# Performance work log

Measured on AMD Instinct MI355X. Metric: run time of the kernel, lower is better.

Reference implementation:

```python
import jax, jax.numpy as jnp
import numpy as np

EPS = 1e-12  # torch F.normalize eps


def setup_inputs() -> dict:
    key = jax.random.key(0)
    ks = jax.random.split(key, 6)
    B, D, F, N, C, L = 4096, 1024, 1024, 8192, 64, 28
    features = jax.random.normal(ks[0], (B, D), dtype=jnp.float32)
    labels = (jax.random.uniform(ks[1], (B, L)) < 0.2).astype(jnp.float32)  # multi-label targets
    g_weight = jax.random.normal(ks[2], (F, D), dtype=jnp.float32) * 0.02  # nn.Linear weight [out,in]
    ex_features = jax.random.normal(ks[3], (N, D), dtype=jnp.float32)
    ex_class_reps = jax.random.uniform(ks[4], (N, C), dtype=jnp.float32) * 2.0 - 1.0
    class_reps = jax.random.uniform(ks[5], (L, C), dtype=jnp.float32) * 2.0 - 1.0
    return {"features": features, "labels": labels, "g_weight": g_weight,
            "ex_features": ex_features, "ex_class_reps": ex_class_reps,
            "class_reps": class_reps, "p_factor": 3}


def _l2norm(x):
    # torch F.normalize(dim=1): x / max(||x||_2, eps)
    n = jnp.sqrt(jnp.sum(x * x, axis=1, keepdims=True))
    return x / jnp.maximum(n, EPS)


def reference(features, labels, g_weight, ex_features, ex_class_reps, class_reps, p_factor):
    # g projection (bias=False)
    f = features @ g_weight.T            # [B, F]
    exf = ex_features @ g_weight.T       # [N, F]
    # cosine similarity: normalized matmul
    s = _l2norm(f) @ _l2norm(exf).T      # [B, N]
    # power-sign activation
    a = jnp.sign(s) * jnp.abs(s) ** p_factor
    # L1 normalize along exemplar axis
    a = a / jnp.maximum(jnp.sum(jnp.abs(a), axis=1, keepdims=True), EPS)
    # exemplar readout
    echo = a @ ex_class_reps             # [B, C]
    # cdist (euclidean) to class representatives -> negative distances as logits
    diff = echo[:, None, :] - class_reps[None, :, :]   # [B, L, C]
    neg_dists = -jnp.sqrt(jnp.sum(diff * diff, axis=-1))  # [B, L]
    # BCEWithLogitsLoss (mean reduction)
    x, y = neg_dists, labels
    loss = jnp.mean(jnp.maximum(x, 0.0) - x * y + jnp.log1p(jnp.exp(-jnp.abs(x))))
    return (loss, neg_dists)
```

## Files before the change

### kernel.cpp

```cpp
#include <hip/hip_runtime.h>
#include <math.h>

#define EPSN 1e-12f

typedef __attribute__((ext_vector_type(8))) short short8;
typedef __attribute__((ext_vector_type(4))) float f32x4;

__device__ __forceinline__ void split_hi_lo(float x, unsigned short& h, unsigned short& l)
{
    unsigned int xb = __float_as_uint(x);
    h = (unsigned short)(xb >> 16);
    float r = x - __uint_as_float(xb & 0xffff0000u);
    l = (unsigned short)(__float_as_uint(r) >> 16);
}

__device__ __forceinline__ unsigned short f2bf_rne(float x)
{
    unsigned int u = __float_as_uint(x);
    unsigned int r = u + 0x7fffu + ((u >> 16) & 1u);
    return (unsigned short)(r >> 16);
}

__device__ __forceinline__ void gload16(const void* g, void* l)
{
    __builtin_amdgcn_global_load_lds(
        (const __attribute__((address_space(1))) void*)g,
        (__attribute__((address_space(3))) void*)l, 16, 0, 0);
}

__device__ __forceinline__ short8 read_frag(const unsigned char* plane, int row, int chunk)
{
    int byte = row * 128 + ((chunk ^ (row & 7)) << 4);
    return *reinterpret_cast<const short8*>(plane + byte);
}

__device__ __forceinline__ void stage_split(const float* __restrict__ src, int K, int k0,
                                            unsigned char* hi_plane, unsigned char* lo_plane,
                                            int tid)
{
#pragma unroll
    for (int q = 0; q < 8; ++q) {
        int idx = tid + q * 256;
        int row = idx >> 4;
        int f4  = idx & 15;
        float4 v = *reinterpret_cast<const float4*>(&src[(size_t)row * K + k0 + f4 * 4]);
        unsigned short h[4], l[4];
        split_hi_lo(v.x, h[0], l[0]);
        split_hi_lo(v.y, h[1], l[1]);
        split_hi_lo(v.z, h[2], l[2]);
        split_hi_lo(v.w, h[3], l[3]);
        int byte = row * 128 + (((f4 >> 1) ^ (row & 7)) << 4) + (f4 & 1) * 8;
        *reinterpret_cast<ushort4*>(hi_plane + byte) = make_ushort4(h[0], h[1], h[2], h[3]);
        *reinterpret_cast<ushort4*>(lo_plane + byte) = make_ushort4(l[0], l[1], l[2], l[3]);
    }
}

__global__ __launch_bounds__(256)
void split_rows(const float* __restrict__ src, unsigned short* __restrict__ dst)
{
    const int row = blockIdx.x, tid = threadIdx.x;
    float4 v = reinterpret_cast<const float4*>(src + (size_t)row * 1024)[tid];
    unsigned short h[4], l[4];
    split_hi_lo(v.x, h[0], l[0]); split_hi_lo(v.y, h[1], l[1]);
    split_hi_lo(v.z, h[2], l[2]); split_hi_lo(v.w, h[3], l[3]);
    unsigned short* R = dst + (size_t)row * 2048;
    *reinterpret_cast<ushort4*>(R + tid * 4)        = make_ushort4(h[0], h[1], h[2], h[3]);
    *reinterpret_cast<ushort4*>(R + 1024 + tid * 4) = make_ushort4(l[0], l[1], l[2], l[3]);
}

__global__ __launch_bounds__(256)
void l2norm_split(float* __restrict__ X)
{
    const int row = blockIdx.x, tid = threadIdx.x;
    float* Xr = X + (size_t)row * 1024;
    float4 v = reinterpret_cast<float4*>(Xr)[tid];
    float s = v.x * v.x + v.y * v.y + v.z * v.z + v.w * v.w;
#pragma unroll
    for (int off = 32; off > 0; off >>= 1) s += __shfl_down(s, off);
    __shared__ float red[4];
    __shared__ float scale_sh;
    if ((tid & 63) == 0) red[tid >> 6] = s;
    __syncthreads();
    if (tid == 0) {
        float n = sqrtf(red[0] + red[1] + red[2] + red[3]);
        scale_sh = 1.f / fmaxf(n, EPSN);
    }
    __syncthreads();
    const float sc = scale_sh;
    v.x *= sc; v.y *= sc; v.z *= sc; v.w *= sc;
    unsigned short h[4], l[4];
    split_hi_lo(v.x, h[0], l[0]); split_hi_lo(v.y, h[1], l[1]);
    split_hi_lo(v.z, h[2], l[2]); split_hi_lo(v.w, h[3], l[3]);
    unsigned short* R = reinterpret_cast<unsigned short*>(Xr);
    *reinterpret_cast<ushort4*>(R + tid * 4)        = make_ushort4(h[0], h[1], h[2], h[3]);
    *reinterpret_cast<ushort4*>(R + 1024 + tid * 4) = make_ushort4(l[0], l[1], l[2], l[3]);
}

__global__ __launch_bounds__(256)
void transpose_exR(const float* __restrict__ exR, unsigned short* __restrict__ exT, int N)
{
    __shared__ unsigned short sm[64][256];
    const int tid = threadIdx.x;
    const int n0 = blockIdx.x * 256;
    const float4* src = reinterpret_cast<const float4*>(exR + (size_t)(n0 + tid) * 64);
#pragma unroll
    for (int q = 0; q < 16; ++q) {
        float4 v = src[q];
        sm[q * 4 + 0][tid] = f2bf_rne(v.x);
        sm[q * 4 + 1][tid] = f2bf_rne(v.y);
        sm[q * 4 + 2][tid] = f2bf_rne(v.z);
        sm[q * 4 + 3][tid] = f2bf_rne(v.w);
    }
    __syncthreads();
#pragma unroll
    for (int j = 0; j < 32; ++j) {
        int idx = tid + j * 256;
        int c = idx >> 7, nl2 = idx & 127;
        *reinterpret_cast<ushort2*>(exT + (size_t)c * N + n0 + nl2 * 2) =
            *reinterpret_cast<const ushort2*>(&sm[c][nl2 * 2]);
    }
}

__global__ __launch_bounds__(256, 2)
void gemm_ps(const unsigned short* __restrict__ spA, const unsigned short* __restrict__ spW,
             float* __restrict__ C, int Nn, int K)
{
    __shared__ __align__(16) unsigned char smem[65536];
    unsigned char* sA_hi = smem;
    unsigned char* sA_lo = smem + 16384;
    unsigned char* sB_hi = smem + 32768;
    unsigned char* sB_lo = smem + 49152;

    const int tid  = threadIdx.x;
    const int lane = tid & 63;
    const int wave = tid >> 6;
    const int wr = wave >> 1, wc = wave & 1;
    const int brow = blockIdx.y * 128;
    const int bcol = blockIdx.x * 128;
    const char* Abase = (const char*)spA + (size_t)brow * 4096;
    const char* Wbase = (const char*)spW + (size_t)bcol * 4096;

    int offA[4];
#pragma unroll
    for (int i = 0; i < 4; ++i) {
        int t = (wave * 4 + i) * 64 + lane;
        int r = t >> 3, c = (t & 7) ^ (r & 7);
        offA[i] = r * 4096 + c * 16;
    }

    f32x4 acc[4][4] = {};

    for (int k0 = 0; k0 < K; k0 += 64) {
        const int k2 = k0 * 2;
#pragma unroll
        for (int i = 0; i < 4; ++i) {
            gload16(Abase + offA[i] + k2,        sA_hi + (wave * 4 + i) * 1024);
            gload16(Abase + offA[i] + 2048 + k2, sA_lo + (wave * 4 + i) * 1024);
            gload16(Wbase + offA[i] + k2,        sB_hi + (wave * 4 + i) * 1024);
            gload16(Wbase + offA[i] + 2048 + k2, sB_lo + (wave * 4 + i) * 1024);
        }
        __syncthreads();
#pragma unroll
        for (int kk = 0; kk < 2; ++kk) {
            const int ch = kk * 4 + (lane >> 4);
            short8 bh[4], bl[4];
#pragma unroll
            for (int fn = 0; fn < 4; ++fn) {
                int rb = wc * 64 + fn * 16 + (lane & 15);
                bh[fn] = read_frag(sB_hi, rb, ch);
                bl[fn] = read_frag(sB_lo, rb, ch);
            }
#pragma unroll
            for (int fm = 0; fm < 4; ++fm) {
                int ra = wr * 64 + fm * 16 + (lane & 15);
                short8 ah = read_frag(sA_hi, ra, ch);
                short8 al = read_frag(sA_lo, ra, ch);
#pragma unroll
                for (int fn = 0; fn < 4; ++fn) {
                    acc[fm][fn] = __builtin_amdgcn_mfma_f32_16x16x32_bf16(ah, bh[fn], acc[fm][fn], 0, 0, 0);
                    acc[fm][fn] = __builtin_amdgcn_mfma_f32_16x16x32_bf16(ah, bl[fn], acc[fm][fn], 0, 0, 0);
                    acc[fm][fn] = __builtin_amdgcn_mfma_f32_16x16x32_bf16(al, bh[fn], acc[fm][fn], 0, 0, 0);
                }
            }
        }
        __syncthreads();
    }

#pragma unroll
    for (int fm = 0; fm < 4; ++fm)
#pragma unroll
        for (int fn = 0; fn < 4; ++fn)
#pragma unroll
            for (int reg = 0; reg < 4; ++reg) {
                int row = brow + wr * 64 + fm * 16 + (lane >> 4) * 4 + reg;
                int col = bcol + wc * 64 + fn * 16 + (lane & 15);
                C[(size_t)row * Nn + col] = acc[fm][fn][reg];
            }
}

__global__ __launch_bounds__(256, 2)
void gemm_w(const float* __restrict__ A, const unsigned short* __restrict__ spW,
            float* __restrict__ C, int Nn, int K)
{
    __shared__ __align__(16) unsigned char smem[65536];
    unsigned char* sA_hi = smem;
    unsigned char* sA_lo = smem + 16384;
    unsigned char* sB_hi = smem + 32768;
    unsigned char* sB_lo = smem + 49152;

    const int tid  = threadIdx.x;
    const int lane = tid & 63;
    const int wave = tid >> 6;
    const int wr = wave >> 1, wc = wave & 1;
    const int brow = blockIdx.y * 128;
    const int bcol = blockIdx.x * 128;
    const float* Abase = A + (size_t)brow * K;
    const char*  Wbase = (const char*)spW + (size_t)bcol * 4096;

    int offW[4];
#pragma unroll
    for (int i = 0; i < 4; ++i) {
        int t = (wave * 4 + i) * 64 + lane;
        int r = t >> 3, c = (t & 7) ^ (r & 7);
        offW[i] = r * 4096 + c * 16;
    }

    f32x4 acc[4][4] = {};

    for (int k0 = 0; k0 < K; k0 += 64) {
        const int k2 = k0 * 2;
#pragma unroll
        for (int i = 0; i < 4; ++i) {
            gload16(Wbase + offW[i] + k2,        sB_hi + (wave * 4 + i) * 1024);
            gload16(Wbase + offW[i] + 2048 + k2, sB_lo + (wave * 4 + i) * 1024);
        }
        stage_split(Abase, K, k0, sA_hi, sA_lo, tid);
        __syncthreads();
#pragma unroll
        for (int kk = 0; kk < 2; ++kk) {
            const int ch = kk * 4 + (lane >> 4);
            short8 bh[4], bl[4];
#pragma unroll
            for (int fn = 0; fn < 4; ++fn) {
                int rb = wc * 64 + fn * 16 + (lane & 15);
                bh[fn] = read_frag(sB_hi, rb, ch);
                bl[fn] = read_frag(sB_lo, rb, ch);
            }
#pragma unroll
            for (int fm = 0; fm < 4; ++fm) {
                int ra = wr * 64 + fm * 16 + (lane & 15);
                short8 ah = read_frag(sA_hi, ra, ch);
                short8 al = read_frag(sA_lo, ra, ch);
#pragma unroll
                for (int fn = 0; fn < 4; ++fn) {
                    acc[fm][fn] = __builtin_amdgcn_mfma_f32_16x16x32_bf16(ah, bh[fn], acc[fm][fn], 0, 0, 0);
                    acc[fm][fn] = __builtin_amdgcn_mfma_f32_16x16x32_bf16(ah, bl[fn], acc[fm][fn], 0, 0, 0);
                    acc[fm][fn] = __builtin_amdgcn_mfma_f32_16x16x32_bf16(al, bh[fn], acc[fm][fn], 0, 0, 0);
                }
            }
        }
        __syncthreads();
    }

#pragma unroll
    for (int fm = 0; fm < 4; ++fm)
#pragma unroll
        for (int fn = 0; fn < 4; ++fn)
#pragma unroll
            for (int reg = 0; reg < 4; ++reg) {
                int row = brow + wr * 64 + fm * 16 + (lane >> 4) * 4 + reg;
                int col = bcol + wc * 64 + fn * 16 + (lane & 15);
                C[(size_t)row * Nn + col] = acc[fm][fn][reg];
            }
}

__global__ __launch_bounds__(256, 2)
void fused_mfma2(const unsigned short* __restrict__ spnF,
                 const unsigned short* __restrict__ spnE,
                 const unsigned short* __restrict__ exT,
                 float* __restrict__ echo,
                 float* __restrict__ rowsum,
                 const int* __restrict__ p_ptr,
                 int N, int K)
{
    __shared__ __align__(16) unsigned char smem[65536];
    unsigned char* sA_hi = smem;
    unsigned char* sA_lo = smem + 16384;
    unsigned char* sB_hi = smem + 32768;
    unsigned char* sB_lo = smem + 49152;
    unsigned char* aS = smem;
    unsigned char* eT = smem + 49152;

    const int tid  = threadIdx.x;
    const int lane = tid & 63;
    const int wave = tid >> 6;
    const int wr = wave >> 1, wc = wave & 1;
    const int brow  = blockIdx.x * 128;
    const int ncol0 = blockIdx.y * 4 * 128;
    const int p = p_ptr[0];
    const char* Af  = (const char*)spnF + (size_t)brow * 4096;
    const char* eTb = (const char*)exT;

    int offA[4], offE[4];
#pragma unroll
    for (int i = 0; i < 4; ++i) {
        int t = (wave * 4 + i) * 64 + lane;
        int r = t >> 3, c = (t & 7) ^ (r & 7);
        offA[i] = r * 4096 + c * 16;
        int cc = t >> 4, chp = t & 15, c2 = chp ^ (cc & 7);
        offE[i] = cc * (2 * N) + c2 * 16;
    }

    f32x4 acc_e[2][4] = {};
    float rsum[4][4] = {};

    for (int nt = 0; nt < 4; ++nt) {
        const int ncol = ncol0 + nt * 128;
        const char* Bn = (const char*)spnE + (size_t)ncol * 4096;

        f32x4 acc[4][4] = {};
        for (int k0 = 0; k0 < K; k0 += 64) {
            const int k2 = k0 * 2;
#pragma unroll
            for (int i = 0; i < 4; ++i) {
                gload16(Af + offA[i] + k2,        sA_hi + (wave * 4 + i) * 1024);
                gload16(Af + offA[i] + 2048 + k2, sA_lo + (wave * 4 + i) * 1024);
                gload16(Bn + offA[i] + k2,        sB_hi + (wave * 4 + i) * 1024);
                gload16(Bn + offA[i] + 2048 + k2, sB_lo + (wave * 4 + i) * 1024);
            }
            __syncthreads();
#pragma unroll
            for (int kk = 0; kk < 2; ++kk) {
                const int ch = kk * 4 + (lane >> 4);
                short8 bh[4], bl[4];
#pragma unroll
                for (int fn2 = 0; fn2 < 4; ++fn2) {
                    int rb = wc * 64 + fn2 * 16 + (lane & 15);
                    bh[fn2] = read_frag(sB_hi, rb, ch);
                    bl[fn2] = read_frag(sB_lo, rb, ch);
                }
#pragma unroll
                for (int fm = 0; fm < 4; ++fm) {
                    int ra = wr * 64 + fm * 16 + (lane & 15);
                    short8 ah = read_frag(sA_hi, ra, ch);
                    short8 al = read_frag(sA_lo, ra, ch);
#pragma unroll
                    for (int fn2 = 0; fn2 < 4; ++fn2) {
                        acc[fm][fn2] = __builtin_amdgcn_mfma_f32_16x16x32_bf16(ah, bh[fn2], acc[fm][fn2], 0, 0, 0);
                        acc[fm][fn2] = __builtin_amdgcn_mfma_f32_16x16x32_bf16(ah, bl[fn2], acc[fm][fn2], 0, 0, 0);
                        acc[fm][fn2] = __builtin_amdgcn_mfma_f32_16x16x32_bf16(al, bh[fn2], acc[fm][fn2], 0, 0, 0);
                    }
                }
            }
            __syncthreads();
        }

#pragma unroll
        for (int i = 0; i < 4; ++i)
            gload16(eTb + offE[i] + ncol * 2, eT + (wave * 4 + i) * 1024);

#pragma unroll
        for (int fm = 0; fm < 4; ++fm)
#pragma unroll
            for (int reg = 0; reg < 4; ++reg) {
                int row = wr * 64 + fm * 16 + (lane >> 4) * 4 + reg;
#pragma unroll
                for (int fn2 = 0; fn2 < 4; ++fn2) {
                    int col = wc * 64 + fn2 * 16 + (lane & 15);
                    float s = acc[fm][fn2][reg];
                    float a;
                    if (p == 3) a = s * s * s;
                    else        a = copysignf(powf(fabsf(s), (float)p), s);
                    rsum[fm][reg] += fabsf(a);
                    int byte = row * 256 + (((col >> 3) ^ (row & 7)) << 4) + (col & 7) * 2;
                    *reinterpret_cast<unsigned short*>(aS + byte) = f2bf_rne(a);
                }
            }
        __syncthreads();

#pragma unroll
        for (int ks = 0; ks < 4; ++ks) {
            const int ch = ks * 4 + (lane >> 4);
            short8 bfr[4];
#pragma unroll
            for (int fn2 = 0; fn2 < 4; ++fn2) {
                int rc = fn2 * 16 + (lane & 15);
                int byte = rc * 256 + ((ch ^ (rc & 7)) << 4);
                bfr[fn2] = *reinterpret_cast<const short8*>(eT + byte);
            }
#pragma unroll
            for (int fm2 = 0; fm2 < 2; ++fm2) {
                int ra = wave * 32 + fm2 * 16 + (lane & 15);
                int byte = ra * 256 + ((ch ^ (ra & 7)) << 4);
                short8 af = *reinterpret_cast<const short8*>(aS + byte);
#pragma unroll
                for (int fn2 = 0; fn2 < 4; ++fn2)
                    acc_e[fm2][fn2] = __builtin_amdgcn_mfma_f32_16x16x32_bf16(af, bfr[fn2], acc_e[fm2][fn2], 0, 0, 0);
            }
        }
        __syncthreads();
    }

#pragma unroll
    for (int fm2 = 0; fm2 < 2; ++fm2)
#pragma unroll
        for (int fn2 = 0; fn2 < 4; ++fn2)
#pragma unroll
            for (int reg = 0; reg < 4; ++reg) {
                int row = brow + wave * 32 + fm2 * 16 + (lane >> 4) * 4 + reg;
                int col = fn2 * 16 + (lane & 15);
                atomicAdd(&echo[(size_t)row * 64 + col], acc_e[fm2][fn2][reg]);
            }

#pragma unroll
    for (int fm = 0; fm < 4; ++fm)
#pragma unroll
        for (int reg = 0; reg < 4; ++reg) {
            float v = rsum[fm][reg];
            v += __shfl_xor(v, 1);
            v += __shfl_xor(v, 2);
            v += __shfl_xor(v, 4);
            v += __shfl_xor(v, 8);
            if ((lane & 15) == 0) {
                int row = brow + wr * 64 + fm * 16 + (lane >> 4) * 4 + reg;
                atomicAdd(&rowsum[row], v);
            }
        }
}

__global__ __launch_bounds__(256)
void finalize_kernel(const float* __restrict__ echo, const float* __restrict__ rowsum,
                     const float* __restrict__ class_reps,
                     const float* __restrict__ labels,
                     float* __restrict__ out,
                     float* __restrict__ loss_acc,
                     int B, int L, int C)
{
    extern __shared__ float cr[];
    const int tid = threadIdx.x;
    for (int i = tid; i < L * C; i += 256) cr[i] = class_reps[i];
    __syncthreads();

    const int row = blockIdx.x * 256 + tid;
    float lsum = 0.f;
    if (row < B) {
        const float inv = 1.f / fmaxf(rowsum[row], EPSN);
        float e[64];
        const float4* er = reinterpret_cast<const float4*>(echo + (size_t)row * 64);
#pragma unroll
        for (int q = 0; q < 16; ++q) {
            float4 v = er[q];
            e[q * 4 + 0] = v.x * inv; e[q * 4 + 1] = v.y * inv;
            e[q * 4 + 2] = v.z * inv; e[q * 4 + 3] = v.w * inv;
        }
        for (int l = 0; l < L; ++l) {
            float d = 0.f;
#pragma unroll
            for (int c = 0; c < 64; ++c) {
                float t = e[c] - cr[l * 64 + c];
                d += t * t;
            }
            float x = -sqrtf(d);
            out[1 + (size_t)row * L + l] = x;
            float y = labels[(size_t)row * L + l];
            lsum += fmaxf(x, 0.f) - x * y + log1pf(expf(-fabsf(x)));
        }
    }
#pragma unroll
    for (int off = 32; off > 0; off >>= 1) lsum += __shfl_down(lsum, off);
    __shared__ float red[4];
    if ((tid & 63) == 0) red[tid >> 6] = lsum;
    __syncthreads();
    if (tid == 0) atomicAdd(loss_acc, red[0] + red[1] + red[2] + red[3]);
}

__global__ void write_loss(const float* __restrict__ loss_acc,
                           float* __restrict__ out, float invBL)
{
    out[0] = loss_acc[0] * invBL;
}

extern "C" void kernel_launch(void* const* d_in, const int* in_sizes, int n_in,
                              void* d_out, int out_size, void* d_ws, size_t ws_size,
                              hipStream_t stream)
{
    const float* features    = (const float*)d_in[0];
    const float* labels      = (const float*)d_in[1];
    const float* g_weight    = (const float*)d_in[2];
    const float* ex_features = (const float*)d_in[3];
    const float* ex_reps     = (const float*)d_in[4];
    const float* class_reps  = (const float*)d_in[5];
    const int*   p_ptr       = (const int*)d_in[6];

    const int D = 1024;
    const int B = in_sizes[0] / D;
    const int F = in_sizes[2] / D;
    const int N = in_sizes[3] / D;
    const int C = in_sizes[4] / N;
    const int L = in_sizes[5] / C;

    char* ws = (char*)d_ws;
    float*          Xf     = (float*)(ws);
    float*          Xe     = (float*)(ws + (size_t)B * 4096);
    unsigned short* sp_w   = (unsigned short*)(ws + (size_t)(B + N) * 4096);
    unsigned short* exT    = (unsigned short*)(ws + (size_t)(B + N + F) * 4096);
    float*          echo   = (float*)(ws + (size_t)(B + N + F) * 4096 + (size_t)64 * N * 2);
    float*          rsums  = echo + (size_t)B * C;
    float*          loss_a = rsums + B;

    size_t base_end = (size_t)(B + N + F) * 4096 + (size_t)64 * N * 2
                    + ((size_t)B * C + B + 4) * 4;
    size_t scratch_off = (base_end + 255) & ~(size_t)255;
    size_t need = scratch_off + (size_t)N * 4096;
    unsigned short* spA = (unsigned short*)(ws + scratch_off);
    const bool use_presplit = (ws_size >= need);

    hipMemsetAsync(echo, 0, (size_t)(B * C + B + 4) * 4, stream);

    split_rows<<<F, 256, 0, stream>>>(g_weight, sp_w);
    transpose_exR<<<N / 256, 256, 0, stream>>>(ex_reps, exT, N);

    if (use_presplit) {
        split_rows<<<N, 256, 0, stream>>>(ex_features, spA);
        {
            dim3 g2(F / 128, N / 128);
            gemm_ps<<<g2, 256, 0, stream>>>(spA, sp_w, Xe, F, D);
        }
        split_rows<<<B, 256, 0, stream>>>(features, spA);
        {
            dim3 g1(F / 128, B / 128);
            gemm_ps<<<g1, 256, 0, stream>>>(spA, sp_w, Xf, F, D);
        }
    } else {
        dim3 g1(F / 128, B / 128);
        gemm_w<<<g1, 256, 0, stream>>>(features, sp_w, Xf, F, D);
        dim3 g2(F / 128, N / 128);
        gemm_w<<<g2, 256, 0, stream>>>(ex_features, sp_w, Xe, F, D);
    }

    l2norm_split<<<B, 256, 0, stream>>>(Xf);
    l2norm_split<<<N, 256, 0, stream>>>(Xe);

    {
        dim3 g(B / 128, 16);
        fused_mfma2<<<g, 256, 0, stream>>>((const unsigned short*)Xf,
                                           (const unsigned short*)Xe,
                                           exT, echo, rsums, p_ptr, N, F);
    }

    {
        dim3 g((B + 255) / 256);
        size_t shb = (size_t)L * C * sizeof(float);
        finalize_kernel<<<g, 256, shb, stream>>>(echo, rsums, class_reps, labels,
                                                 (float*)d_out, loss_a, B, L, C);
    }
    write_loss<<<1, 1, 0, stream>>>(loss_a, (float*)d_out, 1.f / (float)(B * L));
}
```

Measured before the change: 455.7 us.

## Double-buffer LDS staging with K=32 steps in split-bf16 GEMM kernels

Replaces the single-buffered 64-wide K step with two 32-wide LDS buffers in gemm_ps and fused_mfma2. The next tile is prefetched asynchronously while MFMAs run on the current one, and one barrier per step is dropped. The goal is to overlap global-to-LDS loads with compute. The cost is half the K depth per step, so barriers per unit of K stay about the same, plus a new 64-byte row swizzle that could raise LDS bank conflicts. The echo staging area also moves to S+32768, which has to be kept consistent with the epilogue.

```diff
diff --git a/kernel.cpp b/kernel.cpp
--- a/kernel.cpp
+++ b/kernel.cpp
@@ -55,6 +55,62 @@
     }
 }
 
+__device__ __forceinline__ short8 read_frag32(const unsigned char* plane, int row, int ch)
+{
+    int byte = row * 64 + ((ch ^ ((row >> 1) & 3)) << 4);
+    return *reinterpret_cast<const short8*>(plane + byte);
+}
+
+__device__ __forceinline__ void make_off32(int wave, int lane, int off32[2])
+{
+#pragma unroll
+    for (int i = 0; i < 2; ++i) {
+        int t   = (wave * 2 + i) * 64 + lane;
+        int row = t >> 2;
+        int cl  = t & 3;
+        int cg  = cl ^ ((row >> 1) & 3);
+        off32[i] = row * 4096 + cg * 16;
+    }
+}
+
+__device__ __forceinline__ void stage32(const char* Ab, const char* Bb, int k2,
+                                        unsigned char* buf, const int off32[2], int wave)
+{
+#pragma unroll
+    for (int i = 0; i < 2; ++i) {
+        unsigned char* d = buf + (wave * 2 + i) * 1024;
+        gload16(Ab + off32[i] + k2,        d);
+        gload16(Ab + off32[i] + 2048 + k2, d + 8192);
+        gload16(Bb + off32[i] + k2,        d + 16384);
+        gload16(Bb + off32[i] + 2048 + k2, d + 24576);
+    }
+}
+
+__device__ __forceinline__ void compute32(const unsigned char* buf, int lane, int wr, int wc,
+                                          f32x4 acc[4][4])
+{
+    const int ch = lane >> 4;
+    short8 bh[4], bl[4];
+#pragma unroll
+    for (int fn = 0; fn < 4; ++fn) {
+        int rb = wc * 64 + fn * 16 + (lane & 15);
+        bh[fn] = read_frag32(buf + 16384, rb, ch);
+        bl[fn] = read_frag32(buf + 24576, rb, ch);
+    }
+#pragma unroll
+    for (int fm = 0; fm < 4; ++fm) {
+        int ra = wr * 64 + fm * 16 + (lane & 15);
+        short8 ah = read_frag32(buf,        ra, ch);
+        short8 al = read_frag32(buf + 8192, ra, ch);
+#pragma unroll
+        for (int fn = 0; fn < 4; ++fn) {
+            acc[fm][fn] = __builtin_amdgcn_mfma_f32_16x16x32_bf16(ah, bh[fn], acc[fm][fn], 0, 0, 0);
+            acc[fm][fn] = __builtin_amdgcn_mfma_f32_16x16x32_bf16(ah, bl[fn], acc[fm][fn], 0, 0, 0);
+            acc[fm][fn] = __builtin_amdgcn_mfma_f32_16x16x32_bf16(al, bh[fn], acc[fm][fn], 0, 0, 0);
+        }
+    }
+}
+
 __global__ __launch_bounds__(256)
 void split_rows(const float* __restrict__ src, unsigned short* __restrict__ dst)
 {
@@ -125,11 +181,7 @@
 void gemm_ps(const unsigned short* __restrict__ spA, const unsigned short* __restrict__ spW,
              float* __restrict__ C, int Nn, int K)
 {
-    __shared__ __align__(16) unsigned char smem[65536];
-    unsigned char* sA_hi = smem;
-    unsigned char* sA_lo = smem + 16384;
-    unsigned char* sB_hi = smem + 32768;
-    unsigned char* sB_lo = smem + 49152;
+    __shared__ __align__(16) unsigned char S[65536];
 
     const int tid  = threadIdx.x;
     const int lane = tid & 63;
@@ -137,53 +189,24 @@
     const int wr = wave >> 1, wc = wave & 1;
     const int brow = blockIdx.y * 128;
     const int bcol = blockIdx.x * 128;
-    const char* Abase = (const char*)spA + (size_t)brow * 4096;
-    const char* Wbase = (const char*)spW + (size_t)bcol * 4096;
-
-    int offA[4];
-#pragma unroll
-    for (int i = 0; i < 4; ++i) {
-        int t = (wave * 4 + i) * 64 + lane;
-        int r = t >> 3, c = (t & 7) ^ (r & 7);
-        offA[i] = r * 4096 + c * 16;
-    }
+    const char* Ab = (const char*)spA + (size_t)brow * 4096;
+    const char* Wb = (const char*)spW + (size_t)bcol * 4096;
+
+    int off32[2];
+    make_off32(wave, lane, off32);
 
     f32x4 acc[4][4] = {};
-
-    for (int k0 = 0; k0 < K; k0 += 64) {
-        const int k2 = k0 * 2;
-#pragma unroll
-        for (int i = 0; i < 4; ++i) {
-            gload16(Abase + offA[i] + k2,        sA_hi + (wave * 4 + i) * 1024);
-            gload16(Abase + offA[i] + 2048 + k2, sA_lo + (wave * 4 + i) * 1024);
-            gload16(Wbase + offA[i] + k2,        sB_hi + (wave * 4 + i) * 1024);
-            gload16(Wbase + offA[i] + 2048 + k2, sB_lo + (wave * 4 + i) * 1024);
-        }
+    const int nk = K / 32;
+
+    stage32(Ab, Wb, 0, S, off32, wave);
+    __syncthreads();
+    int cur = 0;
+    for (int k = 0; k < nk; ++k) {
+        if (k + 1 < nk)
+            stage32(Ab, Wb, (k + 1) * 64, S + (cur ^ 1) * 32768, off32, wave);
+        compute32(S + cur * 32768, lane, wr, wc, acc);
         __syncthreads();
-#pragma unroll
-        for (int kk = 0; kk < 2; ++kk) {
-            const int ch = kk * 4 + (lane >> 4);
-            short8 bh[4], bl[4];
-#pragma unroll
-            for (int fn = 0; fn < 4; ++fn) {
-                int rb = wc * 64 + fn * 16 + (lane & 15);
-                bh[fn] = read_frag(sB_hi, rb, ch);
-                bl[fn] = read_frag(sB_lo, rb, ch);
-            }
-#pragma unroll
-            for (int fm = 0; fm < 4; ++fm) {
-                int ra = wr * 64 + fm * 16 + (lane & 15);
-                short8 ah = read_frag(sA_hi, ra, ch);
-                short8 al = read_frag(sA_lo, ra, ch);
-#pragma unroll
-                for (int fn = 0; fn < 4; ++fn) {
-                    acc[fm][fn] = __builtin_amdgcn_mfma_f32_16x16x32_bf16(ah, bh[fn], acc[fm][fn], 0, 0, 0);
-                    acc[fm][fn] = __builtin_amdgcn_mfma_f32_16x16x32_bf16(ah, bl[fn], acc[fm][fn], 0, 0, 0);
-                    acc[fm][fn] = __builtin_amdgcn_mfma_f32_16x16x32_bf16(al, bh[fn], acc[fm][fn], 0, 0, 0);
-                }
-            }
-        }
-        __syncthreads();
+        cur ^= 1;
     }
 
 #pragma unroll
@@ -283,13 +306,9 @@
                  const int* __restrict__ p_ptr,
                  int N, int K)
 {
-    __shared__ __align__(16) unsigned char smem[65536];
-    unsigned char* sA_hi = smem;
-    unsigned char* sA_lo = smem + 16384;
-    unsigned char* sB_hi = smem + 32768;
-    unsigned char* sB_lo = smem + 49152;
-    unsigned char* aS = smem;
-    unsigned char* eT = smem + 49152;
+    __shared__ __align__(16) unsigned char S[65536];
+    unsigned char* aS = S;
+    unsigned char* eT = S + 32768;
 
     const int tid  = threadIdx.x;
     const int lane = tid & 63;
@@ -301,58 +320,35 @@
     const char* Af  = (const char*)spnF + (size_t)brow * 4096;
     const char* eTb = (const char*)exT;
 
-    int offA[4], offE[4];
+    int off32[2];
+    make_off32(wave, lane, off32);
+
+    int offE[4];
 #pragma unroll
     for (int i = 0; i < 4; ++i) {
         int t = (wave * 4 + i) * 64 + lane;
-        int r = t >> 3, c = (t & 7) ^ (r & 7);
-        offA[i] = r * 4096 + c * 16;
         int cc = t >> 4, chp = t & 15, c2 = chp ^ (cc & 7);
         offE[i] = cc * (2 * N) + c2 * 16;
     }
 
     f32x4 acc_e[2][4] = {};
     float rsum[4][4] = {};
+    const int nk = K / 32;
 
     for (int nt = 0; nt < 4; ++nt) {
         const int ncol = ncol0 + nt * 128;
         const char* Bn = (const char*)spnE + (size_t)ncol * 4096;
 
         f32x4 acc[4][4] = {};
-        for (int k0 = 0; k0 < K; k0 += 64) {
-            const int k2 = k0 * 2;
-#pragma unroll
-            for (int i = 0; i < 4; ++i) {
-                gload16(Af + offA[i] + k2,        sA_hi + (wave * 4 + i) * 1024);
-                gload16(Af + offA[i] + 2048 + k2, sA_lo + (wave * 4 + i) * 1024);
-                gload16(Bn + offA[i] + k2,        sB_hi + (wave * 4 + i) * 1024);
-                gload16(Bn + offA[i] + 2048 + k2, sB_lo + (wave * 4 + i) * 1024);
-            }
+        stage32(Af, Bn, 0, S, off32, wave);
+        __syncthreads();
+        int cur = 0;
+        for (int k = 0; k < nk; ++k) {
+            if (k + 1 < nk)
+                stage32(Af, Bn, (k + 1) * 64, S + (cur ^ 1) * 32768, off32, wave);
+            compute32(S + cur * 32768, lane, wr, wc, acc);
             __syncthreads();
-#pragma unroll
-            for (int kk = 0; kk < 2; ++kk) {
-                const int ch = kk * 4 + (lane >> 4);
-                short8 bh[4], bl[4];
-#pragma unroll
-                for (int fn2 = 0; fn2 < 4; ++fn2) {
-                    int rb = wc * 64 + fn2 * 16 + (lane & 15);
-                    bh[fn2] = read_frag(sB_hi, rb, ch);
-                    bl[fn2] = read_frag(sB_lo, rb, ch);
-                }
-#pragma unroll
-                for (int fm = 0; fm < 4; ++fm) {
-                    int ra = wr * 64 + fm * 16 + (lane & 15);
-                    short8 ah = read_frag(sA_hi, ra, ch);
-                    short8 al = read_frag(sA_lo, ra, ch);
-#pragma unroll
-                    for (int fn2 = 0; fn2 < 4; ++fn2) {
-                        acc[fm][fn2] = __builtin_amdgcn_mfma_f32_16x16x32_bf16(ah, bh[fn2], acc[fm][fn2], 0, 0, 0);
-                        acc[fm][fn2] = __builtin_amdgcn_mfma_f32_16x16x32_bf16(ah, bl[fn2], acc[fm][fn2], 0, 0, 0);
-                        acc[fm][fn2] = __builtin_amdgcn_mfma_f32_16x16x32_bf16(al, bh[fn2], acc[fm][fn2], 0, 0, 0);
-                    }
-                }
-            }
-            __syncthreads();
+            cur ^= 1;
         }
 
 #pragma unroll
```

New measurement: 458.1 us. About the same (+0.5%).
